# Kernel tuning notes

Hardware: AMD Instinct MI355X
Metric: run time of the kernel (lower is better)

## Reference

```python
import jax, jax.numpy as jnp
import numpy as np

N = 50000      # num nodes
E = 800000     # edges per hypergraph (avg degree 16)
G = 3          # hyper_edge_num
D_IN = 128
D_OUT = 128


def setup_inputs() -> dict:
    key = jax.random.key(0)
    ks = jax.random.split(key, 6)
    company_emb = jax.random.normal(ks[0], (N, D_IN), dtype=jnp.float32)
    # nn.Linear weight [out, in], glorot-ish scaling
    W = jax.random.normal(ks[1], (D_OUT, D_IN), dtype=jnp.float32) / np.sqrt(D_IN).astype(np.float32)
    alpha = jax.random.normal(ks[2], (G, 1), dtype=jnp.float32)
    edge_rows = jax.random.randint(ks[3], (G, E), 0, N, dtype=jnp.int32)
    edge_cols = jax.random.randint(ks[4], (G, E), 0, N, dtype=jnp.int32)
    edge_vals = jax.random.normal(ks[5], (G, E), dtype=jnp.float32)
    return {
        "company_emb": company_emb,
        "W": W,
        "alpha": alpha,
        "edge_rows": edge_rows,
        "edge_cols": edge_cols,
        "edge_vals": edge_vals,
    }


def reference(company_emb, W, alpha, edge_rows, edge_cols, edge_vals):
    # shared dense projection: h = X @ W^T, [N, D_OUT]
    h = company_emb @ W.T

    def spmm(rows, cols, vals):
        # sparse Laplacian (COO) @ h : gather source rows, scale, scatter-add to dest rows
        msg = vals[:, None] * h[cols]                     # [E, D_OUT]
        return jax.ops.segment_sum(msg, rows, num_segments=N)

    aggs = jax.vmap(spmm)(edge_rows, edge_cols, edge_vals)  # [G, N, D_OUT]
    gate = jax.nn.sigmoid(alpha[:, 0])                       # [G]
    # res = sum_g sigmoid(alpha_g) * (L_g @ h)
    return jnp.einsum('g,gnd->nd', gate, aggs)
```

## Files before the change

kernel.cpp:

```cpp
#include <hip/hip_runtime.h>
#include <math.h>

#define NNODES 50000
#define NEDGE  800000
#define NG     3
#define GE     (NG*NEDGE)
#define NBUK   2048
#define OS     (NBUK + 1)
#define CH     9375
#define NBLK   256
#define GBLK   391
#define FGRID  (GBLK + NBLK)
#define STGCAP 1536
#define NPH    7
#define MAXG   175
#define SCAP   2112

typedef __attribute__((ext_vector_type(8))) short bf16x8;
typedef __attribute__((ext_vector_type(4))) float f32x4;

__device__ __forceinline__ unsigned short f2bf(float f) {
    unsigned u = __float_as_uint(f);
    return (unsigned short)((u + 0x7fffu + ((u >> 16) & 1u)) >> 16);
}

__device__ __forceinline__ int bucket_of(unsigned r) {
    return (int)((r * 128u) / 3125u);
}

__global__ __launch_bounds__(512) void k_front(const float* __restrict__ X,
                                               const float* __restrict__ W,
                                               const int* __restrict__ rows,
                                               const int* __restrict__ cols,
                                               const float* __restrict__ vals,
                                               const float* __restrict__ alpha,
                                               unsigned short* __restrict__ hb16,
                                               uint2* __restrict__ out1,
                                               unsigned short* __restrict__ off1) {
    __shared__ __align__(16) char smem[34816];
    const int t = threadIdx.x;

    if (blockIdx.x < GBLK) {
        uint4* Wl = (uint4*)smem;
        for (int i = t; i < 2048; i += 512) {
            const int nt   = i >> 8;
            const int kc   = (i >> 6) & 3;
            const int lane = i & 63;
            const int n  = nt * 16 + (lane & 15);
            const int k0 = kc * 32 + (lane >> 4) * 8;
            const float* src = W + (size_t)n * 128 + k0;
            float4 a = *(const float4*)(src);
            float4 b = *(const float4*)(src + 4);
            unsigned u0 = (unsigned)f2bf(a.x) | ((unsigned)f2bf(a.y) << 16);
            unsigned u1 = (unsigned)f2bf(a.z) | ((unsigned)f2bf(a.w) << 16);
            unsigned u2 = (unsigned)f2bf(b.x) | ((unsigned)f2bf(b.y) << 16);
            unsigned u3 = (unsigned)f2bf(b.z) | ((unsigned)f2bf(b.w) << 16);
            Wl[i] = make_uint4(u0, u1, u2, u3);
        }
        __syncthreads();

        const int w    = t >> 6;
        const int lane = t & 63;
        const int q    = lane >> 4;
        const int ml   = lane & 15;
        const int m0   = blockIdx.x * 128 + w * 16;

        int xr = m0 + ml; if (xr >= NNODES) xr = NNODES - 1;
        const float* xrow = X + (size_t)xr * 128;

        bf16x8 xf[4];
#pragma unroll
        for (int kc = 0; kc < 4; ++kc) {
            const int k0 = kc * 32 + q * 8;
            float4 a = *(const float4*)(xrow + k0);
            float4 b = *(const float4*)(xrow + k0 + 4);
            bf16x8 v;
            v[0] = (short)f2bf(a.x); v[1] = (short)f2bf(a.y);
            v[2] = (short)f2bf(a.z); v[3] = (short)f2bf(a.w);
            v[4] = (short)f2bf(b.x); v[5] = (short)f2bf(b.y);
            v[6] = (short)f2bf(b.z); v[7] = (short)f2bf(b.w);
            xf[kc] = v;
        }

        f32x4 acc[8];
#pragma unroll
        for (int nt = 0; nt < 8; ++nt) acc[nt] = (f32x4){0.f, 0.f, 0.f, 0.f};
#pragma unroll
        for (int nt = 0; nt < 8; ++nt)
#pragma unroll
            for (int kc = 0; kc < 4; ++kc) {
                const bf16x8 wf = *(const bf16x8*)&Wl[(nt * 4 + kc) * 64 + lane];
                acc[nt] = __builtin_amdgcn_mfma_f32_16x16x32_bf16(xf[kc], wf, acc[nt], 0, 0, 0);
            }
        __syncthreads();

        unsigned short* hst = (unsigned short*)smem + w * 2176;
#pragma unroll
        for (int nt = 0; nt < 8; ++nt)
#pragma unroll
            for (int r = 0; r < 4; ++r)
                hst[(q * 4 + r) * 136 + nt * 16 + ml] = f2bf(acc[nt][r]);
        __syncthreads();

#pragma unroll
        for (int i = 0; i < 4; ++i) {
            const int chunk = i * 64 + lane;
            const int lr    = chunk >> 4;
            const int cc    = chunk & 15;
            const int row   = m0 + lr;
            const uint4 v = *(const uint4*)(hst + lr * 136 + cc * 8);
            if (row < NNODES)
                ((uint4*)(hb16 + (size_t)row * 128))[cc] = v;
        }
    } else {
        unsigned short* rnk = (unsigned short*)smem;
        int*            sA  = (int*)(smem + 18752);
        const int bb    = blockIdx.x - GBLK;
        const int start = bb * CH;

        const float g0 = 1.0f / (1.0f + __expf(-alpha[0]));
        const float g1 = 1.0f / (1.0f + __expf(-alpha[1]));
        const float g2 = 1.0f / (1.0f + __expf(-alpha[2]));

#pragma unroll
        for (int j = 0; j < 4; ++j) sA[t + j * 512] = 0;
        __syncthreads();

        for (int k = t; k < CH; k += 512) {
            const int r = rows[start + k];
            rnk[k] = (unsigned short)atomicAdd(&sA[bucket_of((unsigned)r)], 1);
        }
        __syncthreads();

        for (int off = 1; off < 2048; off <<= 1) {
            int v[4];
#pragma unroll
            for (int j = 0; j < 4; ++j) {
                const int i = t + j * 512;
                v[j] = sA[i] + ((i >= off) ? sA[i - off] : 0);
            }
            __syncthreads();
#pragma unroll
            for (int j = 0; j < 4; ++j) sA[t + j * 512] = v[j];
            __syncthreads();
        }

        for (int b = t; b < NBUK; b += 512)
            off1[(size_t)bb * OS + b] = (unsigned short)(b ? sA[b - 1] : 0);
        if (t == 0) off1[(size_t)bb * OS + NBUK] = (unsigned short)sA[NBUK - 1];

        for (int k = t; k < CH; k += 512) {
            const int idx = start + k;
            const int r = rows[idx];
            const int c = cols[idx];
            const float v = vals[idx];
            const float gv = v * (idx < NEDGE ? g0 : (idx < 2 * NEDGE ? g1 : g2));
            const int b = bucket_of((unsigned)r);
            const int pos = (b ? sA[b - 1] : 0) + (int)rnk[k];
            uint2 rec;
            rec.x = ((unsigned)r << 16) | (unsigned)c;
            rec.y = __float_as_uint(gv);
            out1[(size_t)bb * CH + pos] = rec;
        }
    }
}

__global__ __launch_bounds__(512, 8) void k_agg(const unsigned* __restrict__ hbits,
                                                const uint2* __restrict__ out1,
                                                const unsigned short* __restrict__ off1,
                                                float* __restrict__ out) {
    __shared__ __align__(16) uint2          stg[STGCAP];
    __shared__ __align__(16) unsigned short colS[SCAP];
    __shared__ __align__(16) float          valS[SCAP];
    __shared__ int rh[MAXG], grpBase[MAXG + 1], gcur[MAXG];
    __shared__ int sA[512];
    const int t = threadIdx.x;
    const int b = blockIdx.x;

    const int sstart = (b * 3125 + 127) >> 7;
    const int send   = ((b + 1) * 3125 + 127) >> 7;
    const int width  = send - sstart;
    const int ngrp   = NPH * width;

    if (t < MAXG) rh[t] = 0;

    const int seg  = t & 255;
    const int s0f  = off1[(size_t)seg * OS + b];
    const int e0f  = off1[(size_t)seg * OS + b + 1];
    const int lenf = e0f - s0f;
    const int mid  = s0f + ((lenf + 1) >> 1);
    const int half = t >> 8;
    const int s0   = half ? mid : s0f;
    const int e0   = half ? e0f : mid;
    const int len  = e0 - s0;
    sA[t] = len;
    __syncthreads();

    for (int off = 1; off < 512; off <<= 1) {
        const int v = sA[t] + ((t >= off) ? sA[t - off] : 0);
        __syncthreads();
        sA[t] = v;
        __syncthreads();
    }
    const int base = sA[t] - len;
    __syncthreads();

    {
        const uint2* segp = out1 + (size_t)seg * CH;
        int p = base;
        for (int i = s0; i < e0; ++i, ++p) {
            const uint2 rec = segp[i];
            if (p < STGCAP) {
                stg[p] = rec;
                const int lr = (int)(rec.x >> 16) - sstart;
                const int ph = (int)((rec.x & 0xffffu) >> 13);
                atomicAdd(&rh[ph * width + lr], 1);
            }
        }
    }
    __syncthreads();

    if (t < 256) sA[t] = (t < ngrp) ? ((rh[t] + 3) & ~3) : 0;
    __syncthreads();
    for (int off = 1; off < 256; off <<= 1) {
        int v = 0;
        if (t < 256) v = sA[t] + ((t >= off) ? sA[t - off] : 0);
        __syncthreads();
        if (t < 256) sA[t] = v;
        __syncthreads();
    }
    if (t < ngrp) {
        const int pc = (rh[t] + 3) & ~3;
        const int gb = sA[t] - pc;
        grpBase[t] = gb;
        gcur[t]    = gb;
        for (int k = gb + rh[t]; k < gb + pc; ++k) { colS[k] = 0; valS[k] = 0.f; }
    }
    __syncthreads();
    if (t == 0) grpBase[ngrp] = sA[ngrp - 1];
    __syncthreads();

    {
        const int lim = (base + len < STGCAP) ? (base + len) : STGCAP;
        for (int k = base; k < lim; ++k) {
            const uint2 rec = stg[k];
            const int lr = (int)(rec.x >> 16) - sstart;
            const int ph = (int)((rec.x & 0xffffu) >> 13);
            const int pos = atomicAdd(&gcur[ph * width + lr], 1);
            colS[pos] = (unsigned short)(rec.x & 0xffffu);
            valS[pos] = __uint_as_float(rec.y);
        }
    }
    __syncthreads();

    const int w    = t >> 6;
    const int lane = t & 63;
#define GATH(cc) hbits[(((unsigned)(cc)) << 6) | (unsigned)lane]
    float2 acc[4];
#pragma unroll
    for (int ri = 0; ri < 4; ++ri) acc[ri] = make_float2(0.f, 0.f);

    for (int ph = 0; ph < NPH; ++ph) {
#pragma unroll
        for (int ri = 0; ri < 4; ++ri) {
            const int lr = w + ri * 8;
            if (lr < width) {
                const int g = ph * width + lr;
                const int s = grpBase[g];
                const int e = grpBase[g + 1];
                int i = s;
                for (; i + 8 <= e; i += 8) {
                    const uint2  ca = *(const uint2*)&colS[i];
                    const uint2  cb = *(const uint2*)&colS[i + 4];
                    const float4 v0 = *(const float4*)&valS[i];
                    const float4 v1 = *(const float4*)&valS[i + 4];
                    unsigned hb[8];
                    hb[0] = GATH(ca.x & 0xffffu);
                    hb[1] = GATH(ca.x >> 16);
                    hb[2] = GATH(ca.y & 0xffffu);
                    hb[3] = GATH(ca.y >> 16);
                    hb[4] = GATH(cb.x & 0xffffu);
                    hb[5] = GATH(cb.x >> 16);
                    hb[6] = GATH(cb.y & 0xffffu);
                    hb[7] = GATH(cb.y >> 16);
                    const float vv[8] = {v0.x, v0.y, v0.z, v0.w, v1.x, v1.y, v1.z, v1.w};
#pragma unroll
                    for (int j = 0; j < 8; ++j) {
                        acc[ri].x += vv[j] * __uint_as_float(hb[j] << 16);
                        acc[ri].y += vv[j] * __uint_as_float(hb[j] & 0xffff0000u);
                    }
                }
                if (i < e) {
                    const uint2  ca = *(const uint2*)&colS[i];
                    const float4 v0 = *(const float4*)&valS[i];
                    unsigned hb[4];
                    hb[0] = GATH(ca.x & 0xffffu);
                    hb[1] = GATH(ca.x >> 16);
                    hb[2] = GATH(ca.y & 0xffffu);
                    hb[3] = GATH(ca.y >> 16);
                    const float vv[4] = {v0.x, v0.y, v0.z, v0.w};
#pragma unroll
                    for (int j = 0; j < 4; ++j) {
                        acc[ri].x += vv[j] * __uint_as_float(hb[j] << 16);
                        acc[ri].y += vv[j] * __uint_as_float(hb[j] & 0xffff0000u);
                    }
                }
            }
        }
    }
#undef GATH

#pragma unroll
    for (int ri = 0; ri < 4; ++ri) {
        const int lr = w + ri * 8;
        if (lr < width) {
            const int row = sstart + lr;
            ((float2*)out)[(size_t)row * 64 + lane] = acc[ri];
        }
    }
}

extern "C" void kernel_launch(void* const* d_in, const int* in_sizes, int n_in,
                              void* d_out, int out_size, void* d_ws, size_t ws_size,
                              hipStream_t stream) {
    const float* X     = (const float*)d_in[0];
    const float* W     = (const float*)d_in[1];
    const float* alpha = (const float*)d_in[2];
    const int*   rows  = (const int*)d_in[3];
    const int*   cols  = (const int*)d_in[4];
    const float* vals  = (const float*)d_in[5];
    float* out = (float*)d_out;

    char* ws = (char*)d_ws;
    unsigned*       hbits = (unsigned*)(ws + 0);
    unsigned short* hb16  = (unsigned short*)(ws + 0);
    uint2*          out1  = (uint2*)(ws + 12800000);
    unsigned short* off1  = (unsigned short*)(ws + 32000000);

    hipLaunchKernelGGL(k_front, dim3(FGRID), dim3(512), 0, stream,
                       X, W, rows, cols, vals, alpha, hb16, out1, off1);
    hipLaunchKernelGGL(k_agg, dim3(NBUK), dim3(512), 0, stream,
                       hbits, out1, off1, out);
}
```

Before: 217.1 us.

## Fuse front and aggregation kernels into one persistent kernel with grid barrier

Merges the projection/bucketing kernel and the aggregation kernel into a single persistent kernel of 512 blocks. A global atomic-counter barrier separates the two phases, and each block then processes four aggregation buckets in a loop. The bucketing work is rebalanced so that 135 GEMM blocks also handle some edge segments. This removes a kernel launch and the drain/fill gap between the two kernels, but adds a spin barrier, a memset launch, and caps occupancy at 4 blocks per CU with reused shared memory.

```diff
diff --git a/kernel.cpp b/kernel.cpp
--- a/kernel.cpp
+++ b/kernel.cpp
@@ -10,7 +10,7 @@
 #define CH     9375
 #define NBLK   256
 #define GBLK   391
-#define FGRID  (GBLK + NBLK)
+#define GRID   512
 #define STGCAP 1536
 #define NPH    7
 #define MAXG   175
@@ -28,26 +28,31 @@
     return (int)((r * 128u) / 3125u);
 }
 
-__global__ __launch_bounds__(512) void k_front(const float* __restrict__ X,
-                                               const float* __restrict__ W,
-                                               const int* __restrict__ rows,
-                                               const int* __restrict__ cols,
-                                               const float* __restrict__ vals,
-                                               const float* __restrict__ alpha,
-                                               unsigned short* __restrict__ hb16,
-                                               uint2* __restrict__ out1,
-                                               unsigned short* __restrict__ off1) {
+__global__ __launch_bounds__(512, 4) void k_all(const float* __restrict__ X,
+                                                const float* __restrict__ W,
+                                                const int* __restrict__ rows,
+                                                const int* __restrict__ cols,
+                                                const float* __restrict__ vals,
+                                                const float* __restrict__ alpha,
+                                                unsigned short* __restrict__ hb16,
+                                                uint2* __restrict__ out1,
+                                                unsigned short* __restrict__ off1,
+                                                unsigned* __restrict__ ctr,
+                                                float* __restrict__ out) {
     __shared__ __align__(16) char smem[34816];
-    const int t = threadIdx.x;
-
-    if (blockIdx.x < GBLK) {
+    const int t   = threadIdx.x;
+    const int bid = blockIdx.x;
+    const int w    = t >> 6;
+    const int lane = t & 63;
+
+    if (bid < GBLK) {
         uint4* Wl = (uint4*)smem;
         for (int i = t; i < 2048; i += 512) {
-            const int nt   = i >> 8;
-            const int kc   = (i >> 6) & 3;
-            const int lane = i & 63;
-            const int n  = nt * 16 + (lane & 15);
-            const int k0 = kc * 32 + (lane >> 4) * 8;
+            const int nt = i >> 8;
+            const int kc = (i >> 6) & 3;
+            const int ln = i & 63;
+            const int n  = nt * 16 + (ln & 15);
+            const int k0 = kc * 32 + (ln >> 4) * 8;
             const float* src = W + (size_t)n * 128 + k0;
             float4 a = *(const float4*)(src);
             float4 b = *(const float4*)(src + 4);
@@ -59,11 +64,9 @@
         }
         __syncthreads();
 
-        const int w    = t >> 6;
-        const int lane = t & 63;
-        const int q    = lane >> 4;
-        const int ml   = lane & 15;
-        const int m0   = blockIdx.x * 128 + w * 16;
+        const int q  = lane >> 4;
+        const int ml = lane & 15;
+        const int m0 = bid * 128 + w * 16;
 
         int xr = m0 + ml; if (xr >= NNODES) xr = NNODES - 1;
         const float* xrow = X + (size_t)xr * 128;
@@ -112,210 +115,227 @@
             if (row < NNODES)
                 ((uint4*)(hb16 + (size_t)row * 128))[cc] = v;
         }
-    } else {
-        unsigned short* rnk = (unsigned short*)smem;
-        int*            sA  = (int*)(smem + 18752);
-        const int bb    = blockIdx.x - GBLK;
-        const int start = bb * CH;
-
-        const float g0 = 1.0f / (1.0f + __expf(-alpha[0]));
-        const float g1 = 1.0f / (1.0f + __expf(-alpha[1]));
-        const float g2 = 1.0f / (1.0f + __expf(-alpha[2]));
-
-#pragma unroll
-        for (int j = 0; j < 4; ++j) sA[t + j * 512] = 0;
-        __syncthreads();
-
-        for (int k = t; k < CH; k += 512) {
-            const int r = rows[start + k];
-            rnk[k] = (unsigned short)atomicAdd(&sA[bucket_of((unsigned)r)], 1);
-        }
-        __syncthreads();
-
-        for (int off = 1; off < 2048; off <<= 1) {
-            int v[4];
-#pragma unroll
-            for (int j = 0; j < 4; ++j) {
-                const int i = t + j * 512;
-                v[j] = sA[i] + ((i >= off) ? sA[i - off] : 0);
-            }
-            __syncthreads();
-#pragma unroll
-            for (int j = 0; j < 4; ++j) sA[t + j * 512] = v[j];
-            __syncthreads();
-        }
-
-        for (int b = t; b < NBUK; b += 512)
-            off1[(size_t)bb * OS + b] = (unsigned short)(b ? sA[b - 1] : 0);
-        if (t == 0) off1[(size_t)bb * OS + NBUK] = (unsigned short)sA[NBUK - 1];
-
-        for (int k = t; k < CH; k += 512) {
-            const int idx = start + k;
-            const int r = rows[idx];
-            const int c = cols[idx];
-            const float v = vals[idx];
-            const float gv = v * (idx < NEDGE ? g0 : (idx < 2 * NEDGE ? g1 : g2));
-            const int b = bucket_of((unsigned)r);
-            const int pos = (b ? sA[b - 1] : 0) + (int)rnk[k];
-            uint2 rec;
-            rec.x = ((unsigned)r << 16) | (unsigned)c;
-            rec.y = __float_as_uint(gv);
-            out1[(size_t)bb * CH + pos] = rec;
-        }
+        __syncthreads();
     }
-}
-
-__global__ __launch_bounds__(512, 8) void k_agg(const unsigned* __restrict__ hbits,
-                                                const uint2* __restrict__ out1,
-                                                const unsigned short* __restrict__ off1,
-                                                float* __restrict__ out) {
-    __shared__ __align__(16) uint2          stg[STGCAP];
-    __shared__ __align__(16) unsigned short colS[SCAP];
-    __shared__ __align__(16) float          valS[SCAP];
-    __shared__ int rh[MAXG], grpBase[MAXG + 1], gcur[MAXG];
-    __shared__ int sA[512];
-    const int t = threadIdx.x;
-    const int b = blockIdx.x;
-
-    const int sstart = (b * 3125 + 127) >> 7;
-    const int send   = ((b + 1) * 3125 + 127) >> 7;
-    const int width  = send - sstart;
-    const int ngrp   = NPH * width;
-
-    if (t < MAXG) rh[t] = 0;
-
-    const int seg  = t & 255;
-    const int s0f  = off1[(size_t)seg * OS + b];
-    const int e0f  = off1[(size_t)seg * OS + b + 1];
-    const int lenf = e0f - s0f;
-    const int mid  = s0f + ((lenf + 1) >> 1);
-    const int half = t >> 8;
-    const int s0   = half ? mid : s0f;
-    const int e0   = half ? e0f : mid;
-    const int len  = e0 - s0;
-    sA[t] = len;
+
+    {
+        int bb = -1;
+        if (bid >= GBLK)      bb = bid - GBLK;
+        else if (bid < 135)   bb = 121 + bid;
+        if (bb >= 0) {
+            unsigned short* rnk = (unsigned short*)smem;
+            int*            sA  = (int*)(smem + 18752);
+            const int start = bb * CH;
+
+            const float g0 = 1.0f / (1.0f + __expf(-alpha[0]));
+            const float g1 = 1.0f / (1.0f + __expf(-alpha[1]));
+            const float g2 = 1.0f / (1.0f + __expf(-alpha[2]));
+
+#pragma unroll
+            for (int j = 0; j < 4; ++j) sA[t + j * 512] = 0;
+            __syncthreads();
+
+            for (int k = t; k < CH; k += 512) {
+                const int r = rows[start + k];
+                rnk[k] = (unsigned short)atomicAdd(&sA[bucket_of((unsigned)r)], 1);
+            }
+            __syncthreads();
+
+            for (int off = 1; off < 2048; off <<= 1) {
+                int v[4];
+#pragma unroll
+                for (int j = 0; j < 4; ++j) {
+                    const int i = t + j * 512;
+                    v[j] = sA[i] + ((i >= off) ? sA[i - off] : 0);
+                }
+                __syncthreads();
+#pragma unroll
+                for (int j = 0; j < 4; ++j) sA[t + j * 512] = v[j];
+                __syncthreads();
+            }
+
+            for (int b = t; b < NBUK; b += 512)
+                off1[(size_t)bb * OS + b] = (unsigned short)(b ? sA[b - 1] : 0);
+            if (t == 0) off1[(size_t)bb * OS + NBUK] = (unsigned short)sA[NBUK - 1];
+
+            for (int k = t; k < CH; k += 512) {
+                const int idx = start + k;
+                const int r = rows[idx];
+                const int c = cols[idx];
+                const float v = vals[idx];
+                const float gv = v * (idx < NEDGE ? g0 : (idx < 2 * NEDGE ? g1 : g2));
+                const int b = bucket_of((unsigned)r);
+                const int pos = (b ? sA[b - 1] : 0) + (int)rnk[k];
+                uint2 rec;
+                rec.x = ((unsigned)r << 16) | (unsigned)c;
+                rec.y = __float_as_uint(gv);
+                out1[(size_t)bb * CH + pos] = rec;
+            }
+        }
+    }
+
     __syncthreads();
-
-    for (int off = 1; off < 512; off <<= 1) {
-        const int v = sA[t] + ((t >= off) ? sA[t - off] : 0);
-        __syncthreads();
-        sA[t] = v;
-        __syncthreads();
+    if (t == 0) {
+        __threadfence();
+        __hip_atomic_fetch_add(ctr, 1u, __ATOMIC_ACQ_REL, __HIP_MEMORY_SCOPE_AGENT);
+        while (__hip_atomic_load(ctr, __ATOMIC_ACQUIRE, __HIP_MEMORY_SCOPE_AGENT) < (unsigned)GRID) {
+            __builtin_amdgcn_s_sleep(8);
+        }
     }
-    const int base = sA[t] - len;
     __syncthreads();
-
-    {
-        const uint2* segp = out1 + (size_t)seg * CH;
-        int p = base;
-        for (int i = s0; i < e0; ++i, ++p) {
-            const uint2 rec = segp[i];
-            if (p < STGCAP) {
-                stg[p] = rec;
+    __threadfence();
+
+    const unsigned* __restrict__ hbits = (const unsigned*)hb16;
+    uint2*          stg  = (uint2*)smem;
+    unsigned short* colS = (unsigned short*)(smem + 12288);
+    float*          valS = (float*)(smem + 16512);
+    int* rh      = (int*)(smem + 24960);
+    int* grpBase = (int*)(smem + 25664);
+    int* gcur    = (int*)(smem + 26368);
+    int* sA      = (int*)(smem + 27072);
+
+    for (int jb = 0; jb < 4; ++jb) {
+        __syncthreads();
+        const int b = bid + jb * GRID;
+
+        const int sstart = (b * 3125 + 127) >> 7;
+        const int send   = ((b + 1) * 3125 + 127) >> 7;
+        const int width  = send - sstart;
+        const int ngrp   = NPH * width;
+
+        if (t < MAXG) rh[t] = 0;
+
+        const int seg  = t & 255;
+        const int s0f  = off1[(size_t)seg * OS + b];
+        const int e0f  = off1[(size_t)seg * OS + b + 1];
+        const int lenf = e0f - s0f;
+        const int mid  = s0f + ((lenf + 1) >> 1);
+        const int half = t >> 8;
+        const int s0   = half ? mid : s0f;
+        const int e0   = half ? e0f : mid;
+        const int len  = e0 - s0;
+        sA[t] = len;
+        __syncthreads();
+
+        for (int off = 1; off < 512; off <<= 1) {
+            const int v = sA[t] + ((t >= off) ? sA[t - off] : 0);
+            __syncthreads();
+            sA[t] = v;
+            __syncthreads();
+        }
+        const int base = sA[t] - len;
+        __syncthreads();
+
+        {
+            const uint2* segp = out1 + (size_t)seg * CH;
+            int p = base;
+            for (int i = s0; i < e0; ++i, ++p) {
+                const uint2 rec = segp[i];
+                if (p < STGCAP) {
+                    stg[p] = rec;
+                    const int lr = (int)(rec.x >> 16) - sstart;
+                    const int ph = (int)((rec.x & 0xffffu) >> 13);
+                    atomicAdd(&rh[ph * width + lr], 1);
+                }
+            }
+        }
+        __syncthreads();
+
+        if (t < 256) sA[t] = (t < ngrp) ? ((rh[t] + 3) & ~3) : 0;
+        __syncthreads();
+        for (int off = 1; off < 256; off <<= 1) {
+            int v = 0;
+            if (t < 256) v = sA[t] + ((t >= off) ? sA[t - off] : 0);
+            __syncthreads();
+            if (t < 256) sA[t] = v;
+            __syncthreads();
+        }
+        if (t < ngrp) {
+            const int pc = (rh[t] + 3) & ~3;
+            const int gb = sA[t] - pc;
+            grpBase[t] = gb;
+            gcur[t]    = gb;
+            for (int k = gb + rh[t]; k < gb + pc; ++k) { colS[k] = 0; valS[k] = 0.f; }
+        }
+        __syncthreads();
+        if (t == 0) grpBase[ngrp] = sA[ngrp - 1];
+        __syncthreads();
+
+        {
+            const int lim = (base + len < STGCAP) ? (base + len) : STGCAP;
+            for (int k = base; k < lim; ++k) {
+                const uint2 rec = stg[k];
                 const int lr = (int)(rec.x >> 16) - sstart;
                 const int ph = (int)((rec.x & 0xffffu) >> 13);
-                atomicAdd(&rh[ph * width + lr], 1);
-            }
-        }
-    }
-    __syncthreads();
-
-    if (t < 256) sA[t] = (t < ngrp) ? ((rh[t] + 3) & ~3) : 0;
-    __syncthreads();
-    for (int off = 1; off < 256; off <<= 1) {
-        int v = 0;
-        if (t < 256) v = sA[t] + ((t >= off) ? sA[t - off] : 0);
-        __syncthreads();
-        if (t < 256) sA[t] = v;
-        __syncthreads();
-    }
-    if (t < ngrp) {
-        const int pc = (rh[t] + 3) & ~3;
-        const int gb = sA[t] - pc;
-        grpBase[t] = gb;
-        gcur[t]    = gb;
-        for (int k = gb + rh[t]; k < gb + pc; ++k) { colS[k] = 0; valS[k] = 0.f; }
-    }
-    __syncthreads();
-    if (t == 0) grpBase[ngrp] = sA[ngrp - 1];
-    __syncthreads();
-
-    {
-        const int lim = (base + len < STGCAP) ? (base + len) : STGCAP;
-        for (int k = base; k < lim; ++k) {
-            const uint2 rec = stg[k];
-            const int lr = (int)(rec.x >> 16) - sstart;
-            const int ph = (int)((rec.x & 0xffffu) >> 13);
-            const int pos = atomicAdd(&gcur[ph * width + lr], 1);
-            colS[pos] = (unsigned short)(rec.x & 0xffffu);
-            valS[pos] = __uint_as_float(rec.y);
-        }
-    }
-    __syncthreads();
-
-    const int w    = t >> 6;
-    const int lane = t & 63;
+                const int pos = atomicAdd(&gcur[ph * width + lr], 1);
+                colS[pos] = (unsigned short)(rec.x & 0xffffu);
+                valS[pos] = __uint_as_float(rec.y);
+            }
+        }
+        __syncthreads();
+
 #define GATH(cc) hbits[(((unsigned)(cc)) << 6) | (unsigned)lane]
-    float2 acc[4];
-#pragma unroll
-    for (int ri = 0; ri < 4; ++ri) acc[ri] = make_float2(0.f, 0.f);
-
-    for (int ph = 0; ph < NPH; ++ph) {
+        float2 acc[4];
+#pragma unroll
+        for (int ri = 0; ri < 4; ++ri) acc[ri] = make_float2(0.f, 0.f);
+
+        for (int ph = 0; ph < NPH; ++ph) {
+#pragma unroll
+            for (int ri = 0; ri < 4; ++ri) {
+                const int lr = w + ri * 8;
+                if (lr < width) {
+                    const int g = ph * width + lr;
+                    const int s = grpBase[g];
+                    const int e = grpBase[g + 1];
+                    int i = s;
+                    for (; i + 8 <= e; i += 8) {
+                        const uint2  ca = *(const uint2*)&colS[i];
+                        const uint2  cb = *(const uint2*)&colS[i + 4];
+                        const float4 v0 = *(const float4*)&valS[i];
+                        const float4 v1 = *(const float4*)&valS[i + 4];
+                        unsigned hb[8];
+                        hb[0] = GATH(ca.x & 0xffffu);
+                        hb[1] = GATH(ca.x >> 16);
+                        hb[2] = GATH(ca.y & 0xffffu);
+                        hb[3] = GATH(ca.y >> 16);
+                        hb[4] = GATH(cb.x & 0xffffu);
+                        hb[5] = GATH(cb.x >> 16);
+                        hb[6] = GATH(cb.y & 0xffffu);
+                        hb[7] = GATH(cb.y >> 16);
+                        const float vv[8] = {v0.x, v0.y, v0.z, v0.w, v1.x, v1.y, v1.z, v1.w};
+#pragma unroll
+                        for (int j = 0; j < 8; ++j) {
+                            acc[ri].x += vv[j] * __uint_as_float(hb[j] << 16);
+                            acc[ri].y += vv[j] * __uint_as_float(hb[j] & 0xffff0000u);
+                        }
+                    }
+                    if (i < e) {
+                        const uint2  ca = *(const uint2*)&colS[i];
+                        const float4 v0 = *(const float4*)&valS[i];
+                        unsigned hb[4];
+                        hb[0] = GATH(ca.x & 0xffffu);
+                        hb[1] = GATH(ca.x >> 16);
+                        hb[2] = GATH(ca.y & 0xffffu);
+                        hb[3] = GATH(ca.y >> 16);
+                        const float vv[4] = {v0.x, v0.y, v0.z, v0.w};
+#pragma unroll
+                        for (int j = 0; j < 4; ++j) {
+                            acc[ri].x += vv[j] * __uint_as_float(hb[j] << 16);
+                            acc[ri].y += vv[j] * __uint_as_float(hb[j] & 0xffff0000u);
+                        }
+                    }
+                }
+            }
+        }
+#undef GATH
+
 #pragma unroll
         for (int ri = 0; ri < 4; ++ri) {
             const int lr = w + ri * 8;
             if (lr < width) {
-                const int g = ph * width + lr;
-                const int s = grpBase[g];
-                const int e = grpBase[g + 1];
-                int i = s;
-                for (; i + 8 <= e; i += 8) {
-                    const uint2  ca = *(const uint2*)&colS[i];
-                    const uint2  cb = *(const uint2*)&colS[i + 4];
-                    const float4 v0 = *(const float4*)&valS[i];
-                    const float4 v1 = *(const float4*)&valS[i + 4];
-                    unsigned hb[8];
-                    hb[0] = GATH(ca.x & 0xffffu);
-                    hb[1] = GATH(ca.x >> 16);
-                    hb[2] = GATH(ca.y & 0xffffu);
-                    hb[3] = GATH(ca.y >> 16);
-                    hb[4] = GATH(cb.x & 0xffffu);
-                    hb[5] = GATH(cb.x >> 16);
-                    hb[6] = GATH(cb.y & 0xffffu);
-                    hb[7] = GATH(cb.y >> 16);
-                    const float vv[8] = {v0.x, v0.y, v0.z, v0.w, v1.x, v1.y, v1.z, v1.w};
-#pragma unroll
-                    for (int j = 0; j < 8; ++j) {
-                        acc[ri].x += vv[j] * __uint_as_float(hb[j] << 16);
-                        acc[ri].y += vv[j] * __uint_as_float(hb[j] & 0xffff0000u);
-                    }
-                }
-                if (i < e) {
-                    const uint2  ca = *(const uint2*)&colS[i];
-                    const float4 v0 = *(const float4*)&valS[i];
-                    unsigned hb[4];
-                    hb[0] = GATH(ca.x & 0xffffu);
-                    hb[1] = GATH(ca.x >> 16);
-                    hb[2] = GATH(ca.y & 0xffffu);
-                    hb[3] = GATH(ca.y >> 16);
-                    const float vv[4] = {v0.x, v0.y, v0.z, v0.w};
-#pragma unroll
-                    for (int j = 0; j < 4; ++j) {
-                        acc[ri].x += vv[j] * __uint_as_float(hb[j] << 16);
-                        acc[ri].y += vv[j] * __uint_as_float(hb[j] & 0xffff0000u);
-                    }
-                }
-            }
-        }
-    }
-#undef GATH
-
-#pragma unroll
-    for (int ri = 0; ri < 4; ++ri) {
-        const int lr = w + ri * 8;
-        if (lr < width) {
-            const int row = sstart + lr;
-            ((float2*)out)[(size_t)row * 64 + lane] = acc[ri];
+                const int row = sstart + lr;
+                ((float2*)out)[(size_t)row * 64 + lane] = acc[ri];
+            }
         }
     }
 }
@@ -332,13 +352,12 @@
     float* out = (float*)d_out;
 
     char* ws = (char*)d_ws;
-    unsigned*       hbits = (unsigned*)(ws + 0);
-    unsigned short* hb16  = (unsigned short*)(ws + 0);
-    uint2*          out1  = (uint2*)(ws + 12800000);
-    unsigned short* off1  = (unsigned short*)(ws + 32000000);
-
-    hipLaunchKernelGGL(k_front, dim3(FGRID), dim3(512), 0, stream,
-                       X, W, rows, cols, vals, alpha, hb16, out1, off1);
-    hipLaunchKernelGGL(k_agg, dim3(NBUK), dim3(512), 0, stream,
-                       hbits, out1, off1, out);
+    unsigned short* hb16 = (unsigned short*)(ws + 0);
+    uint2*          out1 = (uint2*)(ws + 12800000);
+    unsigned short* off1 = (unsigned short*)(ws + 32000000);
+    unsigned*       ctr  = (unsigned*)(ws + 33049088);
+
+    hipMemsetAsync(ctr, 0, 4, stream);
+    hipLaunchKernelGGL(k_all, dim3(GRID), dim3(512), 0, stream,
+                       X, W, rows, cols, vals, alpha, hb16, out1, off1, ctr, out);
 }
```

Measured after the change: 457.5 us. 111% more time.
